# Kernel tuning notes

Measured on AMD Instinct MI355X. Metric: run time of the kernel, lower is better.

## Reference

```python
import jax, jax.numpy as jnp
import numpy as np


def _rope(x):
    # x: [..., T, hs]
    T, hs = x.shape[-2], x.shape[-1]
    pos = jnp.arange(T, dtype=x.dtype)[:, None]                      # [T,1]
    theta = 1.0 / (10000.0 ** (jnp.arange(0, hs, 2, dtype=x.dtype) / hs))  # [hs/2]
    ang = pos * theta                                                # [T, hs/2]
    cos, sin = jnp.cos(ang), jnp.sin(ang)
    x1, x2 = x[..., 0::2], x[..., 1::2]
    out = jnp.stack([x1 * cos - x2 * sin, x1 * sin + x2 * cos], axis=-1)
    return out.reshape(x.shape)


def _layernorm(x, w, b, eps=1e-5):
    mu = jnp.mean(x, axis=-1, keepdims=True)
    var = jnp.mean(jnp.square(x - mu), axis=-1, keepdims=True)
    return (x - mu) * jax.lax.rsqrt(var + eps) * w + b


def setup_inputs() -> dict:
    key = jax.random.key(0)
    ks = jax.random.split(key, 8)
    B, T, D, H, HS = 8, 1024, 1024, 16, 64
    s = lambda fan: 1.0 / np.sqrt(fan)
    return {
        'x': jax.random.normal(ks[0], (B, T, D), jnp.float32),
        'wq': jax.random.normal(ks[1], (H, D, HS), jnp.float32) * s(D),
        'wk': jax.random.normal(ks[2], (H, D, HS), jnp.float32) * s(D),
        'wv': jax.random.normal(ks[3], (H, D, HS), jnp.float32) * s(D),
        'w_proj': jax.random.normal(ks[4], (D, D), jnp.float32) * s(D),
        'b_proj': jnp.zeros((D,), jnp.float32),
        'ln1_w': jnp.ones((D,), jnp.float32),
        'ln1_b': jnp.zeros((D,), jnp.float32),
        'ln2_w': jnp.ones((D,), jnp.float32),
        'ln2_b': jnp.zeros((D,), jnp.float32),
        'w1': jax.random.normal(ks[5], (D, 4 * D), jnp.float32) * s(D),
        'b1': jnp.zeros((4 * D,), jnp.float32),
        'w2': jax.random.normal(ks[6], (4 * D, D), jnp.float32) * s(4 * D),
        'b2': jnp.zeros((D,), jnp.float32),
    }


def reference(x, wq, wk, wv, w_proj, b_proj, ln1_w, ln1_b, ln2_w, ln2_b, w1, b1, w2, b2):
    B, T, D = x.shape
    H, _, HS = wq.shape
    # --- attention sub-block (pre-LN, causal, RoPE on q/k) ---
    xn = _layernorm(x, ln1_w, ln1_b)
    q = jnp.einsum('btd,hdk->bhtk', xn, wq)   # [B,H,T,HS]
    k = jnp.einsum('btd,hdk->bhtk', xn, wk)
    v = jnp.einsum('btd,hdk->bhtk', xn, wv)
    q = _rope(q)
    k = _rope(k)
    scores = jnp.einsum('bhqk,bhsk->bhqs', q, k) * (HS ** -0.5)  # [B,H,T,T]
    causal = jnp.tril(jnp.ones((T, T), bool))
    scores = jnp.where(causal, scores, -jnp.inf)
    attn = jax.nn.softmax(scores, axis=-1)
    o = jnp.einsum('bhqs,bhsk->bhqk', attn, v)                   # [B,H,T,HS]
    o = jnp.transpose(o, (0, 2, 1, 3)).reshape(B, T, H * HS)     # concat heads
    x = x + o @ w_proj + b_proj                                  # dropout is identity in eval
    # --- FFN sub-block ---
    xn2 = _layernorm(x, ln2_w, ln2_b)
    h = jax.nn.relu(xn2 @ w1 + b1)
    x = x + h @ w2 + b2
    return x
```

## Files before the change

kernel.cpp:

```cpp
#include <hip/hip_runtime.h>
#include <hip/hip_bf16.h>
#include <math.h>

#define DEV static __device__ __forceinline__

typedef __attribute__((ext_vector_type(8))) __bf16 bf16x8;
typedef __attribute__((ext_vector_type(4))) float f32x4;
typedef __attribute__((ext_vector_type(8))) unsigned short ushort8;
typedef __attribute__((ext_vector_type(4))) unsigned short ushort4v;

#define Bb 8
#define Tt 1024
#define Dd 1024
#define Hh 16
#define HS 64
#define BT 8192
#define DFF 4096
#define QS 8388608ull

DEV unsigned short f2bf(float f) {
  union { float f; unsigned int u; } v; v.f = f;
  unsigned int r = v.u + 0x7fffu + ((v.u >> 16) & 1u);
  return (unsigned short)(r >> 16);
}
DEV float bf2f(unsigned short h) {
  union { unsigned int u; float f; } v; v.u = ((unsigned int)h) << 16;
  return v.f;
}

DEV void gload_lds16(const void* g, void* l) {
  __builtin_amdgcn_global_load_lds(
      (const __attribute__((address_space(1))) void*)g,
      (__attribute__((address_space(3))) void*)l, 16, 0, 0);
}

__global__ __launch_bounds__(256) void pack_qkv_t(const float* __restrict__ wq,
                                                  const float* __restrict__ wk,
                                                  const float* __restrict__ wv,
                                                  unsigned short* __restrict__ dst) {
  __shared__ float tile[32][33];
  int z = blockIdx.z, which = z >> 4, hh = z & 15;
  const float* src = which == 0 ? wq : (which == 1 ? wk : wv);
  int d0 = blockIdx.y * 32, hs0 = blockIdx.x * 32;
  int c = threadIdx.x & 31, r8 = threadIdx.x >> 5;
  #pragma unroll
  for (int r = 0; r < 4; ++r) {
    int d = d0 + r8 + r * 8;
    tile[r8 + r * 8][c] = src[((size_t)hh * Dd + d) * HS + hs0 + c];
  }
  __syncthreads();
  #pragma unroll
  for (int r = 0; r < 4; ++r) {
    int hs = hs0 + r8 + r * 8;
    dst[((size_t)which * 1024 + hh * 64 + hs) * Dd + d0 + c] = f2bf(tile[c][r8 + r * 8]);
  }
}

__global__ __launch_bounds__(256) void pack_t_tiled(const float* __restrict__ src,
                                                    unsigned short* __restrict__ dst,
                                                    int N, int K) {
  __shared__ float tile[32][33];
  int n0 = blockIdx.x * 32, k0 = blockIdx.y * 32;
  int c = threadIdx.x & 31, r8 = threadIdx.x >> 5;
  #pragma unroll
  for (int r = 0; r < 4; ++r)
    tile[r8 + r * 8][c] = src[(size_t)(k0 + r8 + r * 8) * N + n0 + c];
  __syncthreads();
  #pragma unroll
  for (int r = 0; r < 4; ++r)
    dst[(size_t)(n0 + r8 + r * 8) * K + k0 + c] = f2bf(tile[c][r8 + r * 8]);
}

__global__ __launch_bounds__(256) void ln_k(const float* __restrict__ in,
                                            const float* __restrict__ w,
                                            const float* __restrict__ b,
                                            unsigned short* __restrict__ out) {
  __shared__ float sbuf[8];
  int row = blockIdx.x, t = threadIdx.x;
  const float4 v = ((const float4*)(in + (size_t)row * Dd))[t];
  float s = v.x + v.y + v.z + v.w;
  float q = v.x * v.x + v.y * v.y + v.z * v.z + v.w * v.w;
  #pragma unroll
  for (int o = 32; o > 0; o >>= 1) { s += __shfl_down(s, o); q += __shfl_down(q, o); }
  if ((t & 63) == 0) { sbuf[t >> 6] = s; sbuf[4 + (t >> 6)] = q; }
  __syncthreads();
  s = (sbuf[0] + sbuf[1]) + (sbuf[2] + sbuf[3]);
  q = (sbuf[4] + sbuf[5]) + (sbuf[6] + sbuf[7]);
  float mu = s * (1.f / Dd);
  float var = q * (1.f / Dd) - mu * mu;
  float inv = rsqrtf(var + 1e-5f);
  const float4 wv = ((const float4*)w)[t];
  const float4 bv = ((const float4*)b)[t];
  ushort4v r;
  r[0] = f2bf((v.x - mu) * inv * wv.x + bv.x);
  r[1] = f2bf((v.y - mu) * inv * wv.y + bv.y);
  r[2] = f2bf((v.z - mu) * inv * wv.z + bv.z);
  r[3] = f2bf((v.w - mu) * inv * wv.w + bv.w);
  *(ushort4v*)&out[(size_t)row * Dd + t * 4] = r;
}

DEV void stage128(const unsigned short* __restrict__ g, int ldK, int k0,
                  unsigned short* lds, int tid) {
  #pragma unroll
  for (int j = 0; j < 2; ++j) {
    int idx = j * 256 + tid;
    int r = idx >> 2, s = idx & 3;
    int sw = (r + (r >> 2)) & 3;
    gload_lds16(g + (size_t)r * ldK + k0 + (((s ^ sw)) * 8), lds + (size_t)idx * 8);
  }
}

template <int MODE>
__global__ __launch_bounds__(256, 4) void gemm_m97(
    const unsigned short* __restrict__ A, const unsigned short* __restrict__ Bt,
    int M, int N, int K,
    const float* __restrict__ resid, const float* __restrict__ bias,
    float* __restrict__ outf, unsigned short* __restrict__ outb) {
  __shared__ __align__(16) unsigned short As[2][128 * 32];
  __shared__ __align__(16) unsigned short Bs[2][128 * 32];
  const int tid = threadIdx.x;
  const int lane = tid & 63, wave = tid >> 6;
  const int l15 = lane & 15, lg = lane >> 4;
  const int wm = wave >> 1, wn = wave & 1;
  const int swr = (l15 + (l15 >> 2)) & 3;

  int nwg = gridDim.x * gridDim.y;
  int orig = blockIdx.y * gridDim.x + blockIdx.x;
  int swz = (orig & 7) * (nwg >> 3) + (orig >> 3);
  int bx = swz % gridDim.x, by = swz / gridDim.x;
  const int brow = by * 128, bcol = bx * 128;

  const unsigned short* Ag = A + (size_t)brow * K;
  const unsigned short* Bg = Bt + (size_t)bcol * K;
  const int NT = K >> 5;

  stage128(Ag, K, 0, As[0], tid);
  stage128(Bg, K, 0, Bs[0], tid);
  asm volatile("s_waitcnt vmcnt(0)" ::: "memory");
  __builtin_amdgcn_s_barrier();

  f32x4 acc[4][4] = {};

  for (int t = 0; t < NT; ++t) {
    const unsigned short* Abuf = As[t & 1];
    const unsigned short* Bbuf = Bs[t & 1];
    if (t + 1 < NT) {
      stage128(Ag, K, (t + 1) * 32, As[(t + 1) & 1], tid);
      stage128(Bg, K, (t + 1) * 32, Bs[(t + 1) & 1], tid);
    }
    bf16x8 af[4], bf[4];
    #pragma unroll
    for (int mi = 0; mi < 4; ++mi)
      af[mi] = *(const bf16x8*)&Abuf[(size_t)(wm * 64 + mi * 16 + l15) * 32 + ((lg ^ swr) * 8)];
    #pragma unroll
    for (int ni = 0; ni < 4; ++ni)
      bf[ni] = *(const bf16x8*)&Bbuf[(size_t)(wn * 64 + ni * 16 + l15) * 32 + ((lg ^ swr) * 8)];
    asm volatile("s_waitcnt lgkmcnt(0)" ::: "memory");
    __builtin_amdgcn_sched_barrier(0);
    __builtin_amdgcn_s_setprio(1);
    #pragma unroll
    for (int mi = 0; mi < 4; ++mi)
      #pragma unroll
      for (int ni = 0; ni < 4; ++ni)
        acc[mi][ni] = __builtin_amdgcn_mfma_f32_16x16x32_bf16(af[mi], bf[ni], acc[mi][ni], 0, 0, 0);
    __builtin_amdgcn_s_setprio(0);
    if (t + 1 < NT) asm volatile("s_waitcnt vmcnt(0)" ::: "memory");
    __builtin_amdgcn_s_barrier();
  }

  #pragma unroll
  for (int m = 0; m < 4; ++m) {
    #pragma unroll
    for (int n = 0; n < 4; ++n) {
      int row0 = brow + wm * 64 + m * 16 + lg * 4;
      int col = bcol + wn * 64 + n * 16 + l15;
      if constexpr (MODE == 0) {
        int b = row0 >> 10, t0 = row0 & 1023;
        int which = col >> 10, rem = col & 1023, hh = rem >> 6, hs = rem & 63;
        if (which == 2) {
          uint2 pk;
          pk.x = (unsigned int)f2bf(acc[m][n][0]) | ((unsigned int)f2bf(acc[m][n][1]) << 16);
          pk.y = (unsigned int)f2bf(acc[m][n][2]) | ((unsigned int)f2bf(acc[m][n][3]) << 16);
          *(uint2*)&outb[2 * QS + ((size_t)(b * Hh + hh) * HS + hs) * Tt + t0] = pk;
        } else {
          #pragma unroll
          for (int r = 0; r < 4; ++r)
            outb[(size_t)which * QS + ((size_t)((b * Hh + hh) * Tt + t0 + r)) * HS + hs] =
                f2bf(acc[m][n][r]);
        }
      } else if constexpr (MODE == 1) {
        #pragma unroll
        for (int r = 0; r < 4; ++r)
          outf[(size_t)(row0 + r) * N + col] =
              resid[(size_t)(row0 + r) * N + col] + acc[m][n][r] + bias[col];
      } else {
        #pragma unroll
        for (int r = 0; r < 4; ++r) {
          float z = acc[m][n][r] + bias[col];
          outb[(size_t)(row0 + r) * N + col] = f2bf(z > 0.f ? z : 0.f);
        }
      }
    }
  }
}

__global__ void rope_k(unsigned short* __restrict__ qkv) {
  int idx = blockIdx.x * 256 + threadIdx.x;
  int which = idx >> 20;
  int rem = idx & 1048575;
  int i8 = rem & 7;
  int t = (rem >> 3) & 1023;
  int bh = rem >> 13;
  unsigned short* p = qkv + (size_t)which * QS + ((size_t)(bh * Tt + t)) * HS + i8 * 8;
  ushort8 v = *(const ushort8*)p;
  float scale = which == 0 ? 0.18033688f : 1.0f;
  ushort8 o;
  #pragma unroll
  for (int e = 0; e < 4; ++e) {
    int i = i8 * 4 + e;
    float theta = exp2f(-(float)i * (13.287712379549449f / 32.f));
    float ang = (float)t * theta;
    float sn, cs;
    __sincosf(ang, &sn, &cs);
    float x1 = bf2f(v[e * 2]), x2 = bf2f(v[e * 2 + 1]);
    o[e * 2]     = f2bf((x1 * cs - x2 * sn) * scale);
    o[e * 2 + 1] = f2bf((x1 * sn + x2 * cs) * scale);
  }
  *(ushort8*)p = o;
}

__global__ __launch_bounds__(256) void attn_k(const unsigned short* __restrict__ qkv,
                                              unsigned short* __restrict__ O) {
  __shared__ __align__(16) unsigned short K_lds[2][64 * 64];
  __shared__ __align__(16) unsigned short Vt_lds[2][64 * 64];
  __shared__ __align__(16) unsigned short P_lds[4][32 * 64];
  const int tid = threadIdx.x;
  const int wave = tid >> 6, lane = tid & 63;
  const int l15 = lane & 15, lg = lane >> 4;
  const int sw = l15 & 7;
  const int bh = blockIdx.x;
  const int q0 = (7 - (int)blockIdx.y) * 128;
  const int qw0 = q0 + wave * 32;

  bf16x8 qf[2][2];
  {
    const unsigned short* Qg = qkv + ((size_t)bh * Tt + qw0 + l15) * HS;
    #pragma unroll
    for (int qi = 0; qi < 2; ++qi)
      #pragma unroll
      for (int dg = 0; dg < 2; ++dg)
        qf[qi][dg] = *(const bf16x8*)&Qg[(size_t)qi * 16 * HS + dg * 32 + lg * 8];
  }
  f32x4 oacc[2][4] = {};
  float m_r[2] = {-1e30f, -1e30f};
  float l_r[2] = {0.f, 0.f};

  const unsigned short* Kg = qkv + QS + (size_t)bh * Tt * HS;
  const unsigned short* Vg = qkv + 2 * QS + (size_t)bh * HS * Tt;

  const int srow = lane >> 3;
  const int scol = ((lane & 7) ^ (srow & 7)) * 8;
  const int i0 = wave * 2, i1 = wave * 2 + 1;

#define STAGE_KV(s0_, buf_)                                                        \
  do {                                                                             \
    gload_lds16(Kg + (size_t)((s0_) + i0 * 8 + srow) * HS + scol,                  \
                (char*)&K_lds[buf_][0] + i0 * 1024);                               \
    gload_lds16(Kg + (size_t)((s0_) + i1 * 8 + srow) * HS + scol,                  \
                (char*)&K_lds[buf_][0] + i1 * 1024);                               \
    gload_lds16(Vg + (size_t)(i0 * 8 + srow) * Tt + (s0_) + scol,                  \
                (char*)&Vt_lds[buf_][0] + i0 * 1024);                              \
    gload_lds16(Vg + (size_t)(i1 * 8 + srow) * Tt + (s0_) + scol,                  \
                (char*)&Vt_lds[buf_][0] + i1 * 1024);                              \
  } while (0)

  const int nsteps = (q0 + 128) >> 6;
  STAGE_KV(0, 0);

  for (int t = 0; t < nsteps; ++t) {
    const int s0 = t << 6;
    if (t + 1 < nsteps) {
      STAGE_KV(s0 + 64, (t + 1) & 1);
      asm volatile("s_waitcnt vmcnt(4)" ::: "memory");
    } else {
      asm volatile("s_waitcnt vmcnt(0)" ::: "memory");
    }
    __builtin_amdgcn_s_barrier();

    const unsigned short* Kb = K_lds[t & 1];
    const unsigned short* Vb = Vt_lds[t & 1];

    if (s0 <= qw0 + 31) {
      f32x4 st[4][2];
      #pragma unroll
      for (int si = 0; si < 4; ++si) {
        bf16x8 kf0 = *(const bf16x8*)&Kb[(size_t)(si * 16 + l15) * 64 + ((lg ^ sw) * 8)];
        bf16x8 kf1 = *(const bf16x8*)&Kb[(size_t)(si * 16 + l15) * 64 + (((4 + lg) ^ sw) * 8)];
        #pragma unroll
        for (int qi = 0; qi < 2; ++qi) {
          f32x4 a = {};
          a = __builtin_amdgcn_mfma_f32_16x16x32_bf16(kf0, qf[qi][0], a, 0, 0, 0);
          a = __builtin_amdgcn_mfma_f32_16x16x32_bf16(kf1, qf[qi][1], a, 0, 0, 0);
          st[si][qi] = a;
        }
      }
      if (s0 + 63 > qw0) {
        #pragma unroll
        for (int si = 0; si < 4; ++si)
          #pragma unroll
          for (int qi = 0; qi < 2; ++qi) {
            int base = (s0 + si * 16 + lg * 4) - (qw0 + qi * 16 + l15);
            #pragma unroll
            for (int r = 0; r < 4; ++r)
              if (base + r > 0) st[si][qi][r] = -1e30f;
          }
      }
      #pragma unroll
      for (int qi = 0; qi < 2; ++qi) {
        float ms[4];
        #pragma unroll
        for (int si = 0; si < 4; ++si)
          ms[si] = fmaxf(fmaxf(st[si][qi][0], st[si][qi][1]),
                         fmaxf(st[si][qi][2], st[si][qi][3]));
        float pm = fmaxf(fmaxf(ms[0], ms[1]), fmaxf(ms[2], ms[3]));
        pm = fmaxf(pm, __shfl_xor(pm, 16));
        pm = fmaxf(pm, __shfl_xor(pm, 32));
        if (__any(pm - m_r[qi] > 8.f)) {
          float mn = fmaxf(m_r[qi], pm);
          float corr = __builtin_amdgcn_exp2f(m_r[qi] - mn);
          m_r[qi] = mn;
          l_r[qi] *= corr;
          #pragma unroll
          for (int r = 0; r < 4; ++r) {
            float c = __shfl(corr, (lane & 48) + lg * 4 + r);
            #pragma unroll
            for (int dj = 0; dj < 4; ++dj) oacc[qi][dj][r] *= c;
          }
        }
        float rs = 0.f;
        #pragma unroll
        for (int si = 0; si < 4; ++si) {
          #pragma unroll
          for (int r = 0; r < 4; ++r) {
            float p = __builtin_amdgcn_exp2f(st[si][qi][r] - m_r[qi]);
            st[si][qi][r] = p;
            rs += p;
          }
        }
        rs += __shfl_xor(rs, 16);
        rs += __shfl_xor(rs, 32);
        l_r[qi] += rs;
        #pragma unroll
        for (int si = 0; si < 4; ++si) {
          uint2 pk;
          asm("v_cvt_pk_bf16_f32 %0, %1, %2"
              : "=v"(pk.x) : "v"(st[si][qi][0]), "v"(st[si][qi][1]));
          asm("v_cvt_pk_bf16_f32 %0, %1, %2"
              : "=v"(pk.y) : "v"(st[si][qi][2]), "v"(st[si][qi][3]));
          int slot = si * 2 + (lg >> 1);
          *(uint2*)&P_lds[wave][(size_t)(qi * 16 + l15) * 64 + ((slot ^ sw) * 8) + (lg & 1) * 4] = pk;
        }
      }
      bf16x8 pf[2][2];
      #pragma unroll
      for (int qi = 0; qi < 2; ++qi)
        #pragma unroll
        for (int sg = 0; sg < 2; ++sg)
          pf[qi][sg] = *(const bf16x8*)&P_lds[wave][(size_t)(qi * 16 + l15) * 64 + (((sg * 4 + lg) ^ sw) * 8)];
      #pragma unroll
      for (int dj = 0; dj < 4; ++dj) {
        bf16x8 vf0 = *(const bf16x8*)&Vb[(size_t)(dj * 16 + l15) * 64 + ((lg ^ sw) * 8)];
        bf16x8 vf1 = *(const bf16x8*)&Vb[(size_t)(dj * 16 + l15) * 64 + (((4 + lg) ^ sw) * 8)];
        #pragma unroll
        for (int qi = 0; qi < 2; ++qi) {
          oacc[qi][dj] = __builtin_amdgcn_mfma_f32_16x16x32_bf16(pf[qi][0], vf0, oacc[qi][dj], 0, 0, 0);
          oacc[qi][dj] = __builtin_amdgcn_mfma_f32_16x16x32_bf16(pf[qi][1], vf1, oacc[qi][dj], 0, 0, 0);
        }
      }
    }
    __builtin_amdgcn_s_barrier();
  }
#undef STAGE_KV

  int b = bh >> 4, hh = bh & 15;
  #pragma unroll
  for (int qi = 0; qi < 2; ++qi) {
    float linv = 1.f / l_r[qi];
    #pragma unroll
    for (int r = 0; r < 4; ++r) {
      float li = __shfl(linv, (lane & 48) + lg * 4 + r);
      int qg = qw0 + qi * 16 + lg * 4 + r;
      unsigned short* Og = O + ((size_t)(b * Tt + qg)) * Dd + hh * HS;
      #pragma unroll
      for (int dj = 0; dj < 4; ++dj)
        Og[dj * 16 + l15] = f2bf(oacc[qi][dj][r] * li);
    }
  }
}

extern "C" void kernel_launch(void* const* d_in, const int* in_sizes, int n_in,
                              void* d_out, int out_size, void* d_ws, size_t ws_size,
                              hipStream_t stream) {
  const float* x      = (const float*)d_in[0];
  const float* wq     = (const float*)d_in[1];
  const float* wk     = (const float*)d_in[2];
  const float* wv     = (const float*)d_in[3];
  const float* w_proj = (const float*)d_in[4];
  const float* b_proj = (const float*)d_in[5];
  const float* ln1_w  = (const float*)d_in[6];
  const float* ln1_b  = (const float*)d_in[7];
  const float* ln2_w  = (const float*)d_in[8];
  const float* ln2_b  = (const float*)d_in[9];
  const float* w1     = (const float*)d_in[10];
  const float* b1     = (const float*)d_in[11];
  const float* w2     = (const float*)d_in[12];
  const float* b2     = (const float*)d_in[13];
  float* out = (float*)d_out;

  char* ws = (char*)d_ws;
  unsigned short* Wt_qkv  = (unsigned short*)(ws + 0);
  unsigned short* Wt_proj = (unsigned short*)(ws + 6291456);
  unsigned short* Wt_1    = (unsigned short*)(ws + 8388608);
  unsigned short* Wt_2    = (unsigned short*)(ws + 16777216);
  float*          x1      = (float*)(ws + 25165824);
  unsigned short* xn      = (unsigned short*)(ws + 58720256);
  unsigned short* qkv     = (unsigned short*)(ws + 75497472);
  unsigned short* O       = (unsigned short*)(ws + 125829120);
  unsigned short* xn2     = O;
  unsigned short* hbuf    = (unsigned short*)(ws + 58720256);

  pack_qkv_t<<<dim3(2, 32, 48), 256, 0, stream>>>(wq, wk, wv, Wt_qkv);
  pack_t_tiled<<<dim3(32, 32), 256, 0, stream>>>(w_proj, Wt_proj, 1024, 1024);
  pack_t_tiled<<<dim3(128, 32), 256, 0, stream>>>(w1, Wt_1, 4096, 1024);
  pack_t_tiled<<<dim3(32, 128), 256, 0, stream>>>(w2, Wt_2, 1024, 4096);

  ln_k<<<BT, 256, 0, stream>>>(x, ln1_w, ln1_b, xn);

  gemm_m97<0><<<dim3(24, 64), 256, 0, stream>>>(xn, Wt_qkv, BT, 3072, 1024,
                                                nullptr, nullptr, nullptr, qkv);
  rope_k<<<8192, 256, 0, stream>>>(qkv);

  attn_k<<<dim3(128, 8), 256, 0, stream>>>(qkv, O);

  gemm_m97<1><<<dim3(8, 64), 256, 0, stream>>>(O, Wt_proj, BT, 1024, 1024,
                                               x, b_proj, x1, nullptr);
  ln_k<<<BT, 256, 0, stream>>>(x1, ln2_w, ln2_b, xn2);

  gemm_m97<2><<<dim3(32, 64), 256, 0, stream>>>(xn2, Wt_1, BT, 4096, 1024,
                                                nullptr, b1, nullptr, hbuf);
  gemm_m97<1><<<dim3(8, 64), 256, 0, stream>>>(hbuf, Wt_2, BT, 1024, 4096,
                                               x1, b2, out, nullptr);
}
```

Baseline: 365.8 us.

## Fuse RoPE into QKV GEMM epilogue and deepen GEMM K-tile to 64

Removes the standalone RoPE kernel by applying rotation and query scaling in the QKV GEMM epilogue. A lane shuffle fetches the partner element, and a precomputed cos/sin table supplies the angles. All GEMMs also move from a 32-wide to a 64-wide K tile with an 8-slot XOR swizzle, which halves the number of barriers per K loop. The cost is doubled LDS use (64KB per block) and the loss of the 4-blocks-per-CU launch bound, so occupancy drops. RoPE is now computed from fp32 accumulators before bf16 rounding.

Result: faster. 343.5 us (-6.1%).

```diff
diff --git a/kernel.cpp b/kernel.cpp
--- a/kernel.cpp
+++ b/kernel.cpp
@@ -32,6 +32,15 @@
   __builtin_amdgcn_global_load_lds(
       (const __attribute__((address_space(1))) void*)g,
       (__attribute__((address_space(3))) void*)l, 16, 0, 0);
+}
+
+__global__ void rope_tab_k(float2* __restrict__ tab) {
+  int idx = blockIdx.x * 256 + threadIdx.x;
+  int t = idx >> 5, i = idx & 31;
+  float theta = exp2f(-(float)i * (13.287712379549449f / 32.f));
+  float sn, cs;
+  sincosf((float)t * theta, &sn, &cs);
+  tab[idx] = make_float2(cs, sn);
 }
 
 __global__ __launch_bounds__(256) void pack_qkv_t(const float* __restrict__ wq,
@@ -99,30 +108,30 @@
   *(ushort4v*)&out[(size_t)row * Dd + t * 4] = r;
 }
 
-DEV void stage128(const unsigned short* __restrict__ g, int ldK, int k0,
-                  unsigned short* lds, int tid) {
-  #pragma unroll
-  for (int j = 0; j < 2; ++j) {
+DEV void stage64(const unsigned short* __restrict__ g, int ldK, int k0,
+                 unsigned short* lds, int tid) {
+  #pragma unroll
+  for (int j = 0; j < 4; ++j) {
     int idx = j * 256 + tid;
-    int r = idx >> 2, s = idx & 3;
-    int sw = (r + (r >> 2)) & 3;
-    gload_lds16(g + (size_t)r * ldK + k0 + (((s ^ sw)) * 8), lds + (size_t)idx * 8);
+    int r = idx >> 3, slot = idx & 7;
+    gload_lds16(g + (size_t)r * ldK + k0 + ((slot ^ (r & 7)) * 8),
+                lds + (size_t)idx * 8);
   }
 }
 
 template <int MODE>
-__global__ __launch_bounds__(256, 4) void gemm_m97(
+__global__ __launch_bounds__(256) void gemm_bk64(
     const unsigned short* __restrict__ A, const unsigned short* __restrict__ Bt,
     int M, int N, int K,
-    const float* __restrict__ resid, const float* __restrict__ bias,
+    const float* __restrict__ bias, const float* __restrict__ resid,
     float* __restrict__ outf, unsigned short* __restrict__ outb) {
-  __shared__ __align__(16) unsigned short As[2][128 * 32];
-  __shared__ __align__(16) unsigned short Bs[2][128 * 32];
+  __shared__ __align__(16) unsigned short As[2][128 * 64];
+  __shared__ __align__(16) unsigned short Bs[2][128 * 64];
   const int tid = threadIdx.x;
   const int lane = tid & 63, wave = tid >> 6;
   const int l15 = lane & 15, lg = lane >> 4;
   const int wm = wave >> 1, wn = wave & 1;
-  const int swr = (l15 + (l15 >> 2)) & 3;
+  const int sw = l15 & 7;
 
   int nwg = gridDim.x * gridDim.y;
   int orig = blockIdx.y * gridDim.x + blockIdx.x;
@@ -132,10 +141,10 @@
 
   const unsigned short* Ag = A + (size_t)brow * K;
   const unsigned short* Bg = Bt + (size_t)bcol * K;
-  const int NT = K >> 5;
-
-  stage128(Ag, K, 0, As[0], tid);
-  stage128(Bg, K, 0, Bs[0], tid);
+  const int NT = K >> 6;
+
+  stage64(Ag, K, 0, As[0], tid);
+  stage64(Bg, K, 0, Bs[0], tid);
   asm volatile("s_waitcnt vmcnt(0)" ::: "memory");
   __builtin_amdgcn_s_barrier();
 
@@ -145,24 +154,34 @@
     const unsigned short* Abuf = As[t & 1];
     const unsigned short* Bbuf = Bs[t & 1];
     if (t + 1 < NT) {
-      stage128(Ag, K, (t + 1) * 32, As[(t + 1) & 1], tid);
-      stage128(Bg, K, (t + 1) * 32, Bs[(t + 1) & 1], tid);
-    }
-    bf16x8 af[4], bf[4];
-    #pragma unroll
-    for (int mi = 0; mi < 4; ++mi)
-      af[mi] = *(const bf16x8*)&Abuf[(size_t)(wm * 64 + mi * 16 + l15) * 32 + ((lg ^ swr) * 8)];
-    #pragma unroll
-    for (int ni = 0; ni < 4; ++ni)
-      bf[ni] = *(const bf16x8*)&Bbuf[(size_t)(wn * 64 + ni * 16 + l15) * 32 + ((lg ^ swr) * 8)];
+      stage64(Ag, K, (t + 1) * 64, As[(t + 1) & 1], tid);
+      stage64(Bg, K, (t + 1) * 64, Bs[(t + 1) & 1], tid);
+    }
+    bf16x8 af[4][2], bf[4][2];
+    #pragma unroll
+    for (int mi = 0; mi < 4; ++mi) {
+      int lr = wm * 64 + mi * 16 + l15;
+      #pragma unroll
+      for (int kk = 0; kk < 2; ++kk)
+        af[mi][kk] = *(const bf16x8*)&Abuf[(size_t)lr * 64 + (((kk * 4 + lg) ^ sw) * 8)];
+    }
+    #pragma unroll
+    for (int ni = 0; ni < 4; ++ni) {
+      int lr = wn * 64 + ni * 16 + l15;
+      #pragma unroll
+      for (int kk = 0; kk < 2; ++kk)
+        bf[ni][kk] = *(const bf16x8*)&Bbuf[(size_t)lr * 64 + (((kk * 4 + lg) ^ sw) * 8)];
+    }
     asm volatile("s_waitcnt lgkmcnt(0)" ::: "memory");
     __builtin_amdgcn_sched_barrier(0);
     __builtin_amdgcn_s_setprio(1);
     #pragma unroll
-    for (int mi = 0; mi < 4; ++mi)
-      #pragma unroll
-      for (int ni = 0; ni < 4; ++ni)
-        acc[mi][ni] = __builtin_amdgcn_mfma_f32_16x16x32_bf16(af[mi], bf[ni], acc[mi][ni], 0, 0, 0);
+    for (int kk = 0; kk < 2; ++kk)
+      #pragma unroll
+      for (int mi = 0; mi < 4; ++mi)
+        #pragma unroll
+        for (int ni = 0; ni < 4; ++ni)
+          acc[mi][ni] = __builtin_amdgcn_mfma_f32_16x16x32_bf16(af[mi][kk], bf[ni][kk], acc[mi][ni], 0, 0, 0);
     __builtin_amdgcn_s_setprio(0);
     if (t + 1 < NT) asm volatile("s_waitcnt vmcnt(0)" ::: "memory");
     __builtin_amdgcn_s_barrier();
@@ -183,10 +202,18 @@
           pk.y = (unsigned int)f2bf(acc[m][n][2]) | ((unsigned int)f2bf(acc[m][n][3]) << 16);
           *(uint2*)&outb[2 * QS + ((size_t)(b * Hh + hh) * HS + hs) * Tt + t0] = pk;
         } else {
+          const float2* tab = (const float2*)bias;
+          float qs = (which == 0) ? 0.18033688f : 1.0f;
+          float sgn = ((hs & 1) == 0) ? -1.0f : 1.0f;
           #pragma unroll
-          for (int r = 0; r < 4; ++r)
+          for (int r = 0; r < 4; ++r) {
+            float own = acc[m][n][r];
+            float partner = __shfl_xor(own, 1);
+            float2 cssn = tab[(size_t)(t0 + r) * 32 + (hs >> 1)];
+            float val = (cssn.x * own + sgn * cssn.y * partner) * qs;
             outb[(size_t)which * QS + ((size_t)((b * Hh + hh) * Tt + t0 + r)) * HS + hs] =
-                f2bf(acc[m][n][r]);
+                f2bf(val);
+          }
         }
       } else if constexpr (MODE == 1) {
         #pragma unroll
@@ -202,31 +229,6 @@
       }
     }
   }
-}
-
-__global__ void rope_k(unsigned short* __restrict__ qkv) {
-  int idx = blockIdx.x * 256 + threadIdx.x;
-  int which = idx >> 20;
-  int rem = idx & 1048575;
-  int i8 = rem & 7;
-  int t = (rem >> 3) & 1023;
-  int bh = rem >> 13;
-  unsigned short* p = qkv + (size_t)which * QS + ((size_t)(bh * Tt + t)) * HS + i8 * 8;
-  ushort8 v = *(const ushort8*)p;
-  float scale = which == 0 ? 0.18033688f : 1.0f;
-  ushort8 o;
-  #pragma unroll
-  for (int e = 0; e < 4; ++e) {
-    int i = i8 * 4 + e;
-    float theta = exp2f(-(float)i * (13.287712379549449f / 32.f));
-    float ang = (float)t * theta;
-    float sn, cs;
-    __sincosf(ang, &sn, &cs);
-    float x1 = bf2f(v[e * 2]), x2 = bf2f(v[e * 2 + 1]);
-    o[e * 2]     = f2bf((x1 * cs - x2 * sn) * scale);
-    o[e * 2 + 1] = f2bf((x1 * sn + x2 * cs) * scale);
-  }
-  *(ushort8*)p = o;
 }
 
 __global__ __launch_bounds__(256) void attn_k(const unsigned short* __restrict__ qkv,
@@ -428,7 +430,9 @@
   unsigned short* O       = (unsigned short*)(ws + 125829120);
   unsigned short* xn2     = O;
   unsigned short* hbuf    = (unsigned short*)(ws + 58720256);
-
+  float*          rtab    = (float*)(ws + 141557760);
+
+  rope_tab_k<<<128, 256, 0, stream>>>((float2*)rtab);
   pack_qkv_t<<<dim3(2, 32, 48), 256, 0, stream>>>(wq, wk, wv, Wt_qkv);
   pack_t_tiled<<<dim3(32, 32), 256, 0, stream>>>(w_proj, Wt_proj, 1024, 1024);
   pack_t_tiled<<<dim3(128, 32), 256, 0, stream>>>(w1, Wt_1, 4096, 1024);
@@ -436,18 +440,17 @@
 
   ln_k<<<BT, 256, 0, stream>>>(x, ln1_w, ln1_b, xn);
 
-  gemm_m97<0><<<dim3(24, 64), 256, 0, stream>>>(xn, Wt_qkv, BT, 3072, 1024,
-                                                nullptr, nullptr, nullptr, qkv);
-  rope_k<<<8192, 256, 0, stream>>>(qkv);
+  gemm_bk64<0><<<dim3(24, 64), 256, 0, stream>>>(xn, Wt_qkv, BT, 3072, 1024,
+                                                 rtab, nullptr, nullptr, qkv);
 
   attn_k<<<dim3(128, 8), 256, 0, stream>>>(qkv, O);
 
-  gemm_m97<1><<<dim3(8, 64), 256, 0, stream>>>(O, Wt_proj, BT, 1024, 1024,
-                                               x, b_proj, x1, nullptr);
+  gemm_bk64<1><<<dim3(8, 64), 256, 0, stream>>>(O, Wt_proj, BT, 1024, 1024,
+                                                b_proj, x, x1, nullptr);
   ln_k<<<BT, 256, 0, stream>>>(x1, ln2_w, ln2_b, xn2);
 
-  gemm_m97<2><<<dim3(32, 64), 256, 0, stream>>>(xn2, Wt_1, BT, 4096, 1024,
-                                                nullptr, b1, nullptr, hbuf);
-  gemm_m97<1><<<dim3(8, 64), 256, 0, stream>>>(hbuf, Wt_2, BT, 1024, 4096,
-                                               x1, b2, out, nullptr);
-}
+  gemm_bk64<2><<<dim3(32, 64), 256, 0, stream>>>(xn2, Wt_1, BT, 4096, 1024,
+                                                 b1, nullptr, nullptr, hbuf);
+  gemm_bk64<1><<<dim3(8, 64), 256, 0, stream>>>(hbuf, Wt_2, BT, 1024, 4096,
+                                                b2, x1, out, nullptr);
+}
```
